# Performance work log

Measured on AMD Instinct MI355X. Metric: run time of the kernel, lower is better.

## Reference

```python
import jax, jax.numpy as jnp
from jax import lax
import numpy as np

S, B = 512, 128
D_MODEL = 512
HID = 256
NUM_LAYERS = 2
VOCAB_SRC = 30000
N_TAGS = 32


def setup_inputs() -> dict:
    key = jax.random.key(0)
    ks = jax.random.split(key, 10)
    s = 0.05
    return {
        "source": jax.random.randint(ks[0], (S, B), 0, VOCAB_SRC),
        "target": jax.random.randint(ks[1], (S, B), 0, N_TAGS),
        "emb": jax.random.normal(ks[2], (VOCAB_SRC, D_MODEL), jnp.float32) * s,
        # stacked LSTM weights: [layer, direction, 4H, in] (in == D_MODEL == 2*HID)
        "W_ih": jax.random.normal(ks[3], (NUM_LAYERS, 2, 4 * HID, D_MODEL), jnp.float32) * s,
        "W_hh": jax.random.normal(ks[4], (NUM_LAYERS, 2, 4 * HID, HID), jnp.float32) * s,
        "b_ih": jax.random.normal(ks[5], (NUM_LAYERS, 2, 4 * HID), jnp.float32) * s,
        "b_hh": jax.random.normal(ks[6], (NUM_LAYERS, 2, 4 * HID), jnp.float32) * s,
        "W_lin": jax.random.normal(ks[7], (N_TAGS, 2 * HID), jnp.float32) * s,
        "b_lin": jax.random.normal(ks[8], (N_TAGS,), jnp.float32) * s,
        "transition": jax.random.uniform(ks[9], (N_TAGS, N_TAGS), jnp.float32),
    }


def _lstm_dir(x, Wih, Whh, bias, reverse):
    # x: [S,B,I]; pre-compute input contribution once
    Bsz = x.shape[1]
    H = Whh.shape[1]
    pre = jnp.einsum('sbi,gi->sbg', x, Wih) + bias  # [S,B,4H]

    def cell(carry, p):
        h, c = carry
        gates = p + h @ Whh.T
        i, f, g, o = jnp.split(gates, 4, axis=-1)  # PyTorch gate order i,f,g,o
        c = jax.nn.sigmoid(f) * c + jax.nn.sigmoid(i) * jnp.tanh(g)
        h = jax.nn.sigmoid(o) * jnp.tanh(c)
        return (h, c), h

    init = (jnp.zeros((Bsz, H), x.dtype), jnp.zeros((Bsz, H), x.dtype))
    _, hs = lax.scan(cell, init, pre, reverse=reverse)
    return hs  # [S,B,H] in original time order


def _forward(source, target, emb, W_ih, W_hh, b_ih, b_hh, W_lin, b_lin, transition):
    d = emb.shape[1]
    x = emb[source] * jnp.sqrt(jnp.asarray(d, jnp.float32))  # [S,B,D]
    for l in range(NUM_LAYERS):
        fwd = _lstm_dir(x, W_ih[l, 0], W_hh[l, 0], b_ih[l, 0] + b_hh[l, 0], reverse=False)
        bwd = _lstm_dir(x, W_ih[l, 1], W_hh[l, 1], b_ih[l, 1] + b_hh[l, 1], reverse=True)
        x = jnp.concatenate([fwd, bwd], axis=-1)  # [S,B,2H]
    logits = jnp.einsum('sbh,th->sbt', x, W_lin) + b_lin  # [S,B,T]

    # CRF partition function: alpha recurrence with fused logsumexp
    def step(alpha, e):
        # alpha: [B,T]; transition[j,k] from j->k; e: emissions at step i [B,T]
        alpha = jax.nn.logsumexp(alpha[:, :, None] + transition[None, :, :], axis=1) + e
        return alpha, None

    alpha, _ = lax.scan(step, logits[0], logits[1:])
    log_z = jax.nn.logsumexp(alpha, axis=1)  # [B]

    # gold path score
    em = jnp.take_along_axis(logits, target[:, :, None], axis=2)[..., 0].sum(axis=0)  # [B]
    tr = transition[target[:-1], target[1:]].sum(axis=0)  # [B]
    return jnp.mean(log_z - em - tr)


def reference(source, target, emb, W_ih, W_hh, b_ih, b_hh, W_lin, b_lin, transition):
    return _forward(source, target, emb, W_ih, W_hh, b_ih, b_hh, W_lin, b_lin, transition)
```

## Files before the change

### kernel.cpp

```cpp
#include <hip/hip_runtime.h>
#include <math.h>

typedef __attribute__((ext_vector_type(8))) short short8;
typedef __attribute__((ext_vector_type(4))) float float4v;
typedef __attribute__((ext_vector_type(8))) int int8v;
typedef unsigned short ushort_t;
typedef unsigned char uchar_t;

#define S_LEN 512
#define BATCH 128
#define DMODEL 512
#define HIDDEN 256
#define NTAGS 32
#define MROWS (S_LEN*BATCH)
#define CHUNK 128
#define NCH (S_LEN/CHUNK)
#define EMB_SCALE 22.62741699796952f

__device__ __forceinline__ float bf2f(ushort_t u){
  union { unsigned int i; float f; } v; v.i = ((unsigned int)u)<<16; return v.f;
}
__device__ __forceinline__ ushort_t f2bf(float f){
  union { float f; unsigned int i; } v; v.f = f;
  unsigned int x = v.i;
  x += 0x7fffu + ((x>>16)&1u);
  return (ushort_t)(x>>16);
}
__device__ __forceinline__ uchar_t f2fp8(float f){
  float a = fabsf(f);
  unsigned int s = (__float_as_uint(f) >> 24) & 0x80u;
  if (a >= 448.f) return (uchar_t)(s | 0x7Eu);
  if (a < 0.015625f){
    unsigned int q = (unsigned int)__float2int_rn(a * 512.0f);
    return (uchar_t)(s | q);
  }
  unsigned int x = __float_as_uint(a);
  x += 0x7FFFFu + ((x >> 20) & 1u);
  int e = (int)((x >> 23) & 0xFFu) - 127;
  unsigned int m = (x >> 20) & 7u;
  if (e > 8) return (uchar_t)(s | 0x7Eu);
  return (uchar_t)(s | ((unsigned)(e + 7) << 3) | m);
}
__device__ __forceinline__ float sigm(float x){ return 1.0f/(1.0f+__expf(-x)); }
__device__ __forceinline__ float tanh_f(float x){ return 2.0f/(1.0f+__expf(-2.0f*x)) - 1.0f; }

#define MFMA(a,b,c) __builtin_amdgcn_mfma_f32_16x16x32_bf16(a,b,c,0,0,0)
#define MFMAMX(a,b,c) __builtin_amdgcn_mfma_scale_f32_16x16x128_f8f6f4( \
    a, b, c, 0, 0, 0, 0x7F7F7F7F, 0, 0x7F7F7F7F)

typedef const __attribute__((address_space(1))) void gas_void;
typedef __attribute__((address_space(3))) void las_void;
__device__ __forceinline__ void gload16(const void* g, void* l){
  __builtin_amdgcn_global_load_lds((gas_void*)g, (las_void*)l, 16, 0, 0);
}

__global__ void k_cvt_bf16(const float* __restrict__ s, ushort_t* __restrict__ d, int n){
  int i = blockIdx.x*blockDim.x + threadIdx.x;
  if(i<n) d[i] = f2bf(s[i]);
}
__global__ void k_cvt_fp8p(const float* __restrict__ s, uchar_t* __restrict__ d, int n){
  int i = blockIdx.x*blockDim.x + threadIdx.x;
  if(i<n){
    int row = i >> 8, q = i & 255;
    int u = ((q >> 5) << 5) + ((q & 1) << 4) + ((q >> 1) & 15);
    d[i] = f2fp8(s[row*256 + u]);
  }
}
__global__ void k_biassum(const float* __restrict__ a, const float* __restrict__ b,
                          float* __restrict__ o, int n){
  int i = blockIdx.x*blockDim.x + threadIdx.x;
  if(i<n) o[i] = a[i]+b[i];
}

__global__ __launch_bounds__(64) void k_embed(const int* __restrict__ src,
                                              const float* __restrict__ emb,
                                              ushort_t* __restrict__ x){
  int row = blockIdx.x;
  int t = threadIdx.x;
  int tok = src[row];
  const float4v* e = (const float4v*)(emb + (size_t)tok*DMODEL + t*8);
  float4v a = e[0], b = e[1];
  short8 o;
  o[0]=(short)f2bf(a[0]*EMB_SCALE); o[1]=(short)f2bf(a[1]*EMB_SCALE);
  o[2]=(short)f2bf(a[2]*EMB_SCALE); o[3]=(short)f2bf(a[3]*EMB_SCALE);
  o[4]=(short)f2bf(b[0]*EMB_SCALE); o[5]=(short)f2bf(b[1]*EMB_SCALE);
  o[6]=(short)f2bf(b[2]*EMB_SCALE); o[7]=(short)f2bf(b[3]*EMB_SCALE);
  *(short8*)(x + (size_t)row*DMODEL + t*8) = o;
}

__global__ __launch_bounds__(256) void k_gemm_band(
    const ushort_t* __restrict__ xin, int t0,
    const ushort_t* __restrict__ WihL,
    const float* __restrict__ bsumL,
    ushort_t* __restrict__ outF,
    ushort_t* __restrict__ outB){
  __shared__ __align__(16) uchar_t smem[32768];
  uchar_t* As = smem;
  uchar_t* Bs = smem + 16384;
  int tid = threadIdx.x;
  int tu = blockIdx.x;
  int by = blockIdx.y;
  int dir = by >> 7, bm = by & 127;
  const uchar_t* Ab = (const uchar_t*)(xin +
      (size_t)(dir ? (S_LEN - t0 - CHUNK) : t0)*BATCH*DMODEL +
      (size_t)bm*128*DMODEL);
  const uchar_t* Wb = (const uchar_t*)(WihL + (size_t)dir*1024*DMODEL);
  ushort_t* Cb = dir ? outB : outF;
  const float* bb = bsumL + dir*1024;

  int lane = tid & 63, w = tid >> 6;
  int wm = w >> 1, wn = w & 1;
  int r = lane & 15, hi = lane >> 4;
  int srow = tid >> 3;
  int sslot = (tid & 7) * 16;
  float4v acc[4][4] = {};

  for(int kt=0; kt<8; ++kt){
    #pragma unroll
    for(int i=0;i<4;++i){
      int row = i*32 + srow;
      int src = sslot ^ ((row & 7) << 4);
      gload16(Ab + (size_t)row*1024 + (size_t)kt*128 + src,
              As + i*4096 + w*1024);
      gload16(Wb + (size_t)(i*256 + tu*32 + srow)*1024 + (size_t)kt*128 + src,
              Bs + i*4096 + w*1024);
    }
    __syncthreads();
    #pragma unroll
    for(int ks=0; ks<2; ++ks){
      int kb = ks*64 + hi*16;
      short8 af[4], bf[4];
      #pragma unroll
      for(int m=0;m<4;++m){
        int row = wm*64 + m*16 + r;
        af[m] = *(const short8*)(As + row*128 + (kb ^ ((row&7)<<4)));
      }
      #pragma unroll
      for(int n=0;n<4;++n){
        int row = wn*64 + n*16 + r;
        bf[n] = *(const short8*)(Bs + row*128 + (kb ^ ((row&7)<<4)));
      }
      #pragma unroll
      for(int m=0;m<4;++m)
        #pragma unroll
        for(int n=0;n<4;++n)
          acc[m][n] = MFMA(af[m], bf[n], acc[m][n]);
    }
    __syncthreads();
  }
  uchar_t* Cs = smem;
  int cc = lane & 15;
  #pragma unroll
  for(int n=0;n<4;++n){
    int rb = wn*64 + n*16 + cc;
    int g = rb >> 5, ul = rb & 31;
    int cl = (ul << 2) | g;
    float bv = bb[g*256 + tu*32 + ul];
    #pragma unroll
    for(int m=0;m<4;++m){
      #pragma unroll
      for(int j=0;j<4;++j){
        int row = wm*64 + m*16 + hi*4 + j;
        *(ushort_t*)&Cs[row*256 + ((cl*2) ^ ((row&7)<<4))] =
            f2bf(acc[m][n][j] + bv);
      }
    }
  }
  __syncthreads();
  #pragma unroll
  for(int p=0;p<8;++p){
    int idx = p*4096 + tid*16;
    int row = idx >> 8, cb = idx & 255;
    short8 v = *(const short8*)&Cs[row*256 + (cb ^ ((row&7)<<4))];
    *(short8*)&Cb[(size_t)(bm*128 + row)*1024 + tu*128 + (cb>>1)] = v;
  }
}

__global__ __launch_bounds__(512,1) void k_scan3(
    const ushort_t* __restrict__ preF,
    const ushort_t* __restrict__ preB,
    const uchar_t* __restrict__ Wq,
    uchar_t* __restrict__ hstate,
    float* __restrict__ cstate,
    ushort_t* __restrict__ xout,
    int t0){
  __shared__ __align__(16) uchar_t hbuf[2][288];
  int bid = blockIdx.x;
  int d = bid >> 7, b = bid & 127;
  int tid = threadIdx.x;
  int w = tid >> 6, lane = tid & 63;
  int lo = lane & 15, hi = lane >> 4;
  int u0 = w*32;

  if(tid < 64)
    *(unsigned int*)&hbuf[0][tid*4] =
      *(const unsigned int*)(hstate + ((size_t)d*BATCH + b)*HIDDEN + tid*4);

  int8v wq[4][2][2];
  const uchar_t* Wd = Wq + (size_t)d*1024*HIDDEN;
  #pragma unroll
  for(int g=0; g<4; ++g)
    #pragma unroll
    for(int uh=0; uh<2; ++uh)
      #pragma unroll
      for(int kt=0; kt<2; ++kt)
        wq[g][uh][kt] = *(const int8v*)
          (Wd + (size_t)(g*256 + u0 + uh*16 + lo)*HIDDEN + kt*128 + hi*32);

  float c[2];
  #pragma unroll
  for(int uh=0; uh<2; ++uh)
    c[uh] = cstate[((size_t)d*BATCH + b)*HIDDEN + u0 + uh*16 + lo];

  const ushort_t* pp = (d ? preB : preF) + (size_t)b*1024;
  ushort4 pc[2], pn[2];
  {
    int br = d ? (CHUNK-1) : 0;
    if(hi==0){
      #pragma unroll
      for(int uh=0; uh<2; ++uh)
        pc[uh] = *(const ushort4*)(pp + (size_t)br*BATCH*1024 + (u0+uh*16+lo)*4);
    }
  }
  __syncthreads();

  for(int sb=0; sb<CHUNK; ++sb){
    int p = sb & 1;
    int sb2 = (sb+1 < CHUNK) ? sb+1 : sb;
    int br2 = d ? (CHUNK-1-sb2) : sb2;
    if(hi==0){
      #pragma unroll
      for(int uh=0; uh<2; ++uh)
        pn[uh] = *(const ushort4*)(pp + (size_t)br2*BATCH*1024 + (u0+uh*16+lo)*4);
    }

    int8v ha0 = {0,0,0,0,0,0,0,0};
    int8v ha1 = {0,0,0,0,0,0,0,0};
    if(lo==0){
      ha0 = *(const int8v*)&hbuf[p][hi*32];
      ha1 = *(const int8v*)&hbuf[p][128 + hi*32];
    }
    float4v acc[4][2] = {};
    #pragma unroll
    for(int g=0; g<4; ++g){
      acc[g][0] = MFMAMX(ha0, wq[g][0][0], acc[g][0]);
      acc[g][1] = MFMAMX(ha0, wq[g][1][0], acc[g][1]);
      acc[g][0] = MFMAMX(ha1, wq[g][0][1], acc[g][0]);
      acc[g][1] = MFMAMX(ha1, wq[g][1][1], acc[g][1]);
    }

    int s = t0 + sb;
    int s_eff = d ? (S_LEN-1-s) : s;
    if(hi==0){
      float hnv[2];
      #pragma unroll
      for(int uh=0; uh<2; ++uh){
        float gi = acc[0][uh][0] + bf2f(pc[uh].x);
        float gf = acc[1][uh][0] + bf2f(pc[uh].y);
        float gg = acc[2][uh][0] + bf2f(pc[uh].z);
        float go = acc[3][uh][0] + bf2f(pc[uh].w);
        float cn = sigm(gf)*c[uh] + sigm(gi)*tanh_f(gg);
        float hn = sigm(go)*tanh_f(cn);
        c[uh] = cn;
        hnv[uh] = hn;
        int u = u0 + uh*16 + lo;
        xout[((size_t)s_eff*BATCH + b)*DMODEL + d*HIDDEN + u] = f2bf(hn);
      }
#if __has_builtin(__builtin_amdgcn_cvt_pk_fp8_f32)
      int pk = __builtin_amdgcn_cvt_pk_fp8_f32(hnv[0], hnv[1], 0, false);
      *(ushort_t*)&hbuf[p^1][u0 + 2*lo] = (ushort_t)pk;
#else
      hbuf[p^1][u0 + 2*lo]     = f2fp8(hnv[0]);
      hbuf[p^1][u0 + 2*lo + 1] = f2fp8(hnv[1]);
#endif
    }
    asm volatile("s_waitcnt lgkmcnt(0)\n\ts_barrier" ::: "memory");
    #pragma unroll
    for(int uh=0; uh<2; ++uh) pc[uh] = pn[uh];
  }

  if(tid < 64)
    *(unsigned int*)(hstate + ((size_t)d*BATCH + b)*HIDDEN + tid*4) =
      *(const unsigned int*)&hbuf[0][tid*4];
  if(hi==0){
    #pragma unroll
    for(int uh=0; uh<2; ++uh)
      cstate[((size_t)d*BATCH + b)*HIDDEN + u0 + uh*16 + lo] = c[uh];
  }
}

__global__ __launch_bounds__(256) void k_logits(const ushort_t* __restrict__ x,
                                                const ushort_t* __restrict__ Wl,
                                                const float* __restrict__ bl,
                                                float* __restrict__ logits){
  int tid = threadIdx.x;
  int lane = tid & 63, w = tid >> 6;
  int rowb = blockIdx.x*64 + w*16;
  int r = lane & 15, hi = lane >> 4;
  float4v acc[2] = {};
  #pragma unroll
  for(int kt=0; kt<16; ++kt){
    short8 a  = *(const short8*)&x [(size_t)(rowb + r)*DMODEL + kt*32 + hi*8];
    short8 b0 = *(const short8*)&Wl[(size_t)(r     )*DMODEL + kt*32 + hi*8];
    short8 b1 = *(const short8*)&Wl[(size_t)(16 + r)*DMODEL + kt*32 + hi*8];
    acc[0] = MFMA(a, b0, acc[0]);
    acc[1] = MFMA(a, b1, acc[1]);
  }
  #pragma unroll
  for(int nt=0; nt<2; ++nt){
    float bv = bl[nt*16 + r];
    #pragma unroll
    for(int j=0; j<4; ++j)
      logits[(size_t)(rowb + hi*4 + j)*NTAGS + nt*16 + r] = acc[nt][j] + bv;
  }
}

__global__ __launch_bounds__(64) void k_crf(const float* __restrict__ logits,
                                            const float* __restrict__ trans,
                                            float* __restrict__ logz){
  __shared__ __align__(16) float sh[32];
  int b = blockIdx.x, tid = threadIdx.x;
  int t = tid & 31;

  float eT[32];
  #pragma unroll
  for(int j=0;j<32;++j) eT[j] = __expf(trans[j*NTAGS + t]);

  float al0 = logits[(size_t)b*NTAGS + t];
  float m0 = al0;
  #pragma unroll
  for(int o=1;o<32;o<<=1) m0 = fmaxf(m0, __shfl_xor(m0, o));
  float Mf = m0;
  float a = __expf(al0 - m0);

  const size_t stp = (size_t)BATCH*NTAGS;
  const float* ebase = logits + (size_t)b*NTAGS + t;
  float eCur = ebase[stp*1];
  float eNxt = ebase[stp*2];
  const float* eptr = ebase + stp*3;

  for(int i=1;i<S_LEN;++i){
    float expE = __expf(eCur);
    if(tid < 32) sh[t] = a;
    __syncthreads();
    float eP = 0.f;
    if(i+2 < S_LEN) eP = *eptr;
    eptr += stp;
    float s0=0.f, s1=0.f, s2=0.f, s3=0.f;
    const float4v* s4 = (const float4v*)sh;
    #pragma unroll
    for(int q=0;q<8;++q){
      float4v v = s4[q];
      s0 = __fmaf_rn(v[0], eT[q*4+0], s0);
      s1 = __fmaf_rn(v[1], eT[q*4+1], s1);
      s2 = __fmaf_rn(v[2], eT[q*4+2], s2);
      s3 = __fmaf_rn(v[3], eT[q*4+3], s3);
    }
    a = ((s0+s1)+(s2+s3)) * expE;
    eCur = eNxt; eNxt = eP;
    if(__any(a > 1.1529215e18f) || __all(a < 9.0949470e-13f)){
      float m = a;
      #pragma unroll
      for(int o=1;o<32;o<<=1) m = fmaxf(m, __shfl_xor(m, o));
      int e2 = (int)((__float_as_uint(m)>>23)&255u) - 127;
      float scl = __uint_as_float((unsigned)(127 - e2) << 23);
      a *= scl;
      Mf += (float)e2 * 0.69314718055994531f;
    }
    __syncthreads();
  }
  float sum = a;
  #pragma unroll
  for(int o=1;o<32;o<<=1) sum += __shfl_xor(sum, o);
  if(tid==0) logz[b] = Mf + __logf(sum);
}

__global__ __launch_bounds__(256) void k_gold(const float* __restrict__ logits,
                                              const int* __restrict__ tgt,
                                              const float* __restrict__ trans,
                                              const float* __restrict__ logz,
                                              float* __restrict__ partial){
  int b = blockIdx.x, tid = threadIdx.x;
  float local = 0.f;
  for(int s=tid; s<S_LEN; s+=256){
    int ts = tgt[s*BATCH + b];
    local += logits[((size_t)s*BATCH + b)*NTAGS + ts];
    if(s > 0){
      int tp = tgt[(s-1)*BATCH + b];
      local += trans[tp*NTAGS + ts];
    }
  }
  __shared__ float red[4];
  for(int o=32;o>0;o>>=1) local += __shfl_down(local, o, 64);
  if((tid&63)==0) red[tid>>6] = local;
  __syncthreads();
  if(tid==0) partial[b] = logz[b] - (red[0]+red[1]+red[2]+red[3]);
}
__global__ __launch_bounds__(128) void k_final(const float* __restrict__ partial,
                                               float* __restrict__ out){
  int t = threadIdx.x;
  float v = partial[t];
  for(int o=32;o>0;o>>=1) v += __shfl_down(v, o, 64);
  __shared__ float r2[2];
  if((t&63)==0) r2[t>>6] = v;
  __syncthreads();
  if(t==0) out[0] = (r2[0]+r2[1]) * (1.0f/BATCH);
}

extern "C" void kernel_launch(void* const* d_in, const int* in_sizes, int n_in,
                              void* d_out, int out_size, void* d_ws, size_t ws_size,
                              hipStream_t stream){
  const int*   src   = (const int*)d_in[0];
  const int*   tgt   = (const int*)d_in[1];
  const float* emb   = (const float*)d_in[2];
  const float* Wih   = (const float*)d_in[3];
  const float* Whh   = (const float*)d_in[4];
  const float* bih   = (const float*)d_in[5];
  const float* bhh   = (const float*)d_in[6];
  const float* Wlin  = (const float*)d_in[7];
  const float* blin  = (const float*)d_in[8];
  const float* trans = (const float*)d_in[9];
  float* out = (float*)d_out;
  char* ws = (char*)d_ws;

  ushort_t* xA     = (ushort_t*)(ws + 0);
  ushort_t* xB     = (ushort_t*)(ws + 67108864);
  ushort_t* preF   = (ushort_t*)(ws + 134217728);
  ushort_t* preB   = (ushort_t*)(ws + 167772160);
  ushort_t* WihB   = (ushort_t*)(ws + 201326592);
  uchar_t*  Wq8    = (uchar_t*) (ws + 205520896);
  ushort_t* WlinB  = (ushort_t*)(ws + 206569472);
  float*    bsum   = (float*)   (ws + 206602240);
  uchar_t*  hstate = (uchar_t*) (ws + 206618624);
  float*    cstate = (float*)   (ws + 206684160);
  float*    logz   = (float*)   (ws + 206946304);
  float*    partial= (float*)   (ws + 206946816);
  float*    logits = (float*)   (ws + 134217728);

  k_cvt_bf16<<<dim3(8192),dim3(256),0,stream>>>(Wih,  WihB,  2*2*1024*512);
  k_cvt_fp8p<<<dim3(4096),dim3(256),0,stream>>>(Whh,  Wq8,   2*2*1024*256);
  k_cvt_bf16<<<dim3(64),  dim3(256),0,stream>>>(Wlin, WlinB, 32*512);
  k_biassum <<<dim3(16),  dim3(256),0,stream>>>(bih, bhh, bsum, 2*2*1024);

  k_embed<<<dim3(MROWS),dim3(64),0,stream>>>(src, emb, xA);

  for(int l=0;l<2;++l){
    const ushort_t* xin = l ? xB : xA;
    ushort_t*      xo   = l ? xA : xB;
    hipMemsetAsync(hstate, 0, 65536 + 262144, stream);
    const uchar_t*  WqL   = Wq8  + (size_t)l*2*1024*HIDDEN;
    const ushort_t* WihL  = WihB + (size_t)l*2*1024*DMODEL;
    const float*    bsumL = bsum + l*2*1024;
    for(int c=0;c<NCH;++c){
      int t0 = c*CHUNK;
      k_gemm_band<<<dim3(8, 256),dim3(256),0,stream>>>(
          xin, t0, WihL, bsumL, preF, preB);
      k_scan3<<<dim3(256),dim3(512),0,stream>>>(
          preF, preB, WqL, hstate, cstate, xo, t0);
    }
  }

  k_logits<<<dim3(MROWS/64),dim3(256),0,stream>>>(xA, WlinB, blin, logits);
  k_crf   <<<dim3(BATCH),dim3(64),0,stream>>>(logits, trans, logz);
  k_gold  <<<dim3(BATCH),dim3(256),0,stream>>>(logits, tgt, trans, logz, partial);
  k_final <<<dim3(1),dim3(128),0,stream>>>(partial, out);
}
```

Before: 2.126 ms.

## Overlap next-chunk input GEMM with LSTM scan in one fused launch

Merges the per-chunk input-projection GEMM and the recurrent scan into a single kernel. The first 256 blocks run the sequential LSTM scan on the current chunk while the extra blocks compute the next chunk's pre-activations into a double-buffered band. Only the first band is computed by a standalone GEMM launch. The chunk size is halved to shorten the serial prologue, at the cost of more launches and co-scheduling contention between GEMM and scan blocks.

Measured after the change: 2.296 ms. +8.0%, slower.

```diff
diff --git a/kernel.cpp b/kernel.cpp
--- a/kernel.cpp
+++ b/kernel.cpp
@@ -13,7 +13,7 @@
 #define HIDDEN 256
 #define NTAGS 32
 #define MROWS (S_LEN*BATCH)
-#define CHUNK 128
+#define CHUNK 64
 #define NCH (S_LEN/CHUNK)
 #define EMB_SCALE 22.62741699796952f
 
@@ -99,8 +99,8 @@
   uchar_t* Bs = smem + 16384;
   int tid = threadIdx.x;
   int tu = blockIdx.x;
-  int by = blockIdx.y;
-  int dir = by >> 7, bm = by & 127;
+  int bm = blockIdx.y;
+  int dir = blockIdx.z;
   const uchar_t* Ab = (const uchar_t*)(xin +
       (size_t)(dir ? (S_LEN - t0 - CHUNK) : t0)*BATCH*DMODEL +
       (size_t)bm*128*DMODEL);
@@ -176,116 +176,207 @@
   }
 }
 
-__global__ __launch_bounds__(512,1) void k_scan3(
+__global__ __launch_bounds__(512,1) void k_scan_gemm(
     const ushort_t* __restrict__ preF,
     const ushort_t* __restrict__ preB,
     const uchar_t* __restrict__ Wq,
     uchar_t* __restrict__ hstate,
     float* __restrict__ cstate,
     ushort_t* __restrict__ xout,
-    int t0){
-  __shared__ __align__(16) uchar_t hbuf[2][288];
+    int t0,
+    const ushort_t* __restrict__ xin,
+    const ushort_t* __restrict__ WihL,
+    const float* __restrict__ bsumL,
+    ushort_t* __restrict__ outF,
+    ushort_t* __restrict__ outB,
+    int t0n){
+  __shared__ __align__(16) uchar_t smem[32768];
   int bid = blockIdx.x;
-  int d = bid >> 7, b = bid & 127;
   int tid = threadIdx.x;
-  int w = tid >> 6, lane = tid & 63;
-  int lo = lane & 15, hi = lane >> 4;
-  int u0 = w*32;
-
-  if(tid < 64)
-    *(unsigned int*)&hbuf[0][tid*4] =
-      *(const unsigned int*)(hstate + ((size_t)d*BATCH + b)*HIDDEN + tid*4);
-
-  int8v wq[4][2][2];
-  const uchar_t* Wd = Wq + (size_t)d*1024*HIDDEN;
-  #pragma unroll
-  for(int g=0; g<4; ++g)
+
+  if(bid < 256){
+    uchar_t (*hbuf)[288] = (uchar_t(*)[288])smem;
+    int d = bid >> 7, b = bid & 127;
+    int w = tid >> 6, lane = tid & 63;
+    int lo = lane & 15, hi = lane >> 4;
+    int u0 = w*32;
+
+    if(tid < 64)
+      *(unsigned int*)&hbuf[0][tid*4] =
+        *(const unsigned int*)(hstate + ((size_t)d*BATCH + b)*HIDDEN + tid*4);
+
+    int8v wq[4][2][2];
+    const uchar_t* Wd = Wq + (size_t)d*1024*HIDDEN;
+    #pragma unroll
+    for(int g=0; g<4; ++g)
+      #pragma unroll
+      for(int uh=0; uh<2; ++uh)
+        #pragma unroll
+        for(int kt=0; kt<2; ++kt)
+          wq[g][uh][kt] = *(const int8v*)
+            (Wd + (size_t)(g*256 + u0 + uh*16 + lo)*HIDDEN + kt*128 + hi*32);
+
+    float c[2];
     #pragma unroll
     for(int uh=0; uh<2; ++uh)
-      #pragma unroll
-      for(int kt=0; kt<2; ++kt)
-        wq[g][uh][kt] = *(const int8v*)
-          (Wd + (size_t)(g*256 + u0 + uh*16 + lo)*HIDDEN + kt*128 + hi*32);
-
-  float c[2];
-  #pragma unroll
-  for(int uh=0; uh<2; ++uh)
-    c[uh] = cstate[((size_t)d*BATCH + b)*HIDDEN + u0 + uh*16 + lo];
-
-  const ushort_t* pp = (d ? preB : preF) + (size_t)b*1024;
-  ushort4 pc[2], pn[2];
-  {
-    int br = d ? (CHUNK-1) : 0;
+      c[uh] = cstate[((size_t)d*BATCH + b)*HIDDEN + u0 + uh*16 + lo];
+
+    const ushort_t* pp = (d ? preB : preF) + (size_t)b*1024;
+    ushort4 pc[2], pn[2];
+    {
+      int br = d ? (CHUNK-1) : 0;
+      if(hi==0){
+        #pragma unroll
+        for(int uh=0; uh<2; ++uh)
+          pc[uh] = *(const ushort4*)(pp + (size_t)br*BATCH*1024 + (u0+uh*16+lo)*4);
+      }
+    }
+    __syncthreads();
+
+    for(int sb=0; sb<CHUNK; ++sb){
+      int p = sb & 1;
+      int sb2 = (sb+1 < CHUNK) ? sb+1 : sb;
+      int br2 = d ? (CHUNK-1-sb2) : sb2;
+      if(hi==0){
+        #pragma unroll
+        for(int uh=0; uh<2; ++uh)
+          pn[uh] = *(const ushort4*)(pp + (size_t)br2*BATCH*1024 + (u0+uh*16+lo)*4);
+      }
+
+      int8v ha0 = {0,0,0,0,0,0,0,0};
+      int8v ha1 = {0,0,0,0,0,0,0,0};
+      if(lo==0){
+        ha0 = *(const int8v*)&hbuf[p][hi*32];
+        ha1 = *(const int8v*)&hbuf[p][128 + hi*32];
+      }
+      float4v acc[4][2] = {};
+      #pragma unroll
+      for(int g=0; g<4; ++g){
+        acc[g][0] = MFMAMX(ha0, wq[g][0][0], acc[g][0]);
+        acc[g][1] = MFMAMX(ha0, wq[g][1][0], acc[g][1]);
+        acc[g][0] = MFMAMX(ha1, wq[g][0][1], acc[g][0]);
+        acc[g][1] = MFMAMX(ha1, wq[g][1][1], acc[g][1]);
+      }
+
+      int s = t0 + sb;
+      int s_eff = d ? (S_LEN-1-s) : s;
+      if(hi==0){
+        float hnv[2];
+        #pragma unroll
+        for(int uh=0; uh<2; ++uh){
+          float gi = acc[0][uh][0] + bf2f(pc[uh].x);
+          float gf = acc[1][uh][0] + bf2f(pc[uh].y);
+          float gg = acc[2][uh][0] + bf2f(pc[uh].z);
+          float go = acc[3][uh][0] + bf2f(pc[uh].w);
+          float cn = sigm(gf)*c[uh] + sigm(gi)*tanh_f(gg);
+          float hn = sigm(go)*tanh_f(cn);
+          c[uh] = cn;
+          hnv[uh] = hn;
+          int u = u0 + uh*16 + lo;
+          xout[((size_t)s_eff*BATCH + b)*DMODEL + d*HIDDEN + u] = f2bf(hn);
+        }
+#if __has_builtin(__builtin_amdgcn_cvt_pk_fp8_f32)
+        int pk = __builtin_amdgcn_cvt_pk_fp8_f32(hnv[0], hnv[1], 0, false);
+        *(ushort_t*)&hbuf[p^1][u0 + 2*lo] = (ushort_t)pk;
+#else
+        hbuf[p^1][u0 + 2*lo]     = f2fp8(hnv[0]);
+        hbuf[p^1][u0 + 2*lo + 1] = f2fp8(hnv[1]);
+#endif
+      }
+      asm volatile("s_waitcnt lgkmcnt(0)\n\ts_barrier" ::: "memory");
+      #pragma unroll
+      for(int uh=0; uh<2; ++uh) pc[uh] = pn[uh];
+    }
+
+    if(tid < 64)
+      *(unsigned int*)(hstate + ((size_t)d*BATCH + b)*HIDDEN + tid*4) =
+        *(const unsigned int*)&hbuf[0][tid*4];
     if(hi==0){
       #pragma unroll
       for(int uh=0; uh<2; ++uh)
-        pc[uh] = *(const ushort4*)(pp + (size_t)br*BATCH*1024 + (u0+uh*16+lo)*4);
-    }
-  }
-  __syncthreads();
-
-  for(int sb=0; sb<CHUNK; ++sb){
-    int p = sb & 1;
-    int sb2 = (sb+1 < CHUNK) ? sb+1 : sb;
-    int br2 = d ? (CHUNK-1-sb2) : sb2;
-    if(hi==0){
-      #pragma unroll
-      for(int uh=0; uh<2; ++uh)
-        pn[uh] = *(const ushort4*)(pp + (size_t)br2*BATCH*1024 + (u0+uh*16+lo)*4);
-    }
-
-    int8v ha0 = {0,0,0,0,0,0,0,0};
-    int8v ha1 = {0,0,0,0,0,0,0,0};
-    if(lo==0){
-      ha0 = *(const int8v*)&hbuf[p][hi*32];
-      ha1 = *(const int8v*)&hbuf[p][128 + hi*32];
-    }
+        cstate[((size_t)d*BATCH + b)*HIDDEN + u0 + uh*16 + lo] = c[uh];
+    }
+  } else {
+    int gid = bid - 256;
+    int tu  = gid & 7;
+    int rest = gid >> 3;
+    int dir = rest >> 6, bm = rest & 63;
+    uchar_t* As = smem;
+    uchar_t* Bs = smem + 16384;
+    const uchar_t* Ab = (const uchar_t*)(xin +
+        (size_t)(dir ? (S_LEN - t0n - CHUNK) : t0n)*BATCH*DMODEL +
+        (size_t)bm*128*DMODEL);
+    const uchar_t* Wb = (const uchar_t*)(WihL + (size_t)dir*1024*DMODEL);
+    ushort_t* Cb = dir ? outB : outF;
+    const float* bb = bsumL + dir*1024;
+
+    int lane = tid & 63, w = tid >> 6;
+    int wm = w >> 2, wn = w & 3;
+    int r = lane & 15, hi = lane >> 4;
+    int srow = tid >> 3;
+    int sslot = (tid & 7) * 16;
     float4v acc[4][2] = {};
-    #pragma unroll
-    for(int g=0; g<4; ++g){
-      acc[g][0] = MFMAMX(ha0, wq[g][0][0], acc[g][0]);
-      acc[g][1] = MFMAMX(ha0, wq[g][1][0], acc[g][1]);
-      acc[g][0] = MFMAMX(ha1, wq[g][0][1], acc[g][0]);
-      acc[g][1] = MFMAMX(ha1, wq[g][1][1], acc[g][1]);
-    }
-
-    int s = t0 + sb;
-    int s_eff = d ? (S_LEN-1-s) : s;
-    if(hi==0){
-      float hnv[2];
-      #pragma unroll
-      for(int uh=0; uh<2; ++uh){
-        float gi = acc[0][uh][0] + bf2f(pc[uh].x);
-        float gf = acc[1][uh][0] + bf2f(pc[uh].y);
-        float gg = acc[2][uh][0] + bf2f(pc[uh].z);
-        float go = acc[3][uh][0] + bf2f(pc[uh].w);
-        float cn = sigm(gf)*c[uh] + sigm(gi)*tanh_f(gg);
-        float hn = sigm(go)*tanh_f(cn);
-        c[uh] = cn;
-        hnv[uh] = hn;
-        int u = u0 + uh*16 + lo;
-        xout[((size_t)s_eff*BATCH + b)*DMODEL + d*HIDDEN + u] = f2bf(hn);
-      }
-#if __has_builtin(__builtin_amdgcn_cvt_pk_fp8_f32)
-      int pk = __builtin_amdgcn_cvt_pk_fp8_f32(hnv[0], hnv[1], 0, false);
-      *(ushort_t*)&hbuf[p^1][u0 + 2*lo] = (ushort_t)pk;
-#else
-      hbuf[p^1][u0 + 2*lo]     = f2fp8(hnv[0]);
-      hbuf[p^1][u0 + 2*lo + 1] = f2fp8(hnv[1]);
-#endif
-    }
-    asm volatile("s_waitcnt lgkmcnt(0)\n\ts_barrier" ::: "memory");
-    #pragma unroll
-    for(int uh=0; uh<2; ++uh) pc[uh] = pn[uh];
-  }
-
-  if(tid < 64)
-    *(unsigned int*)(hstate + ((size_t)d*BATCH + b)*HIDDEN + tid*4) =
-      *(const unsigned int*)&hbuf[0][tid*4];
-  if(hi==0){
-    #pragma unroll
-    for(int uh=0; uh<2; ++uh)
-      cstate[((size_t)d*BATCH + b)*HIDDEN + u0 + uh*16 + lo] = c[uh];
+
+    for(int kt=0; kt<8; ++kt){
+      #pragma unroll
+      for(int i=0;i<2;++i){
+        int row = i*64 + srow;
+        int src = sslot ^ ((row & 7) << 4);
+        gload16(Ab + (size_t)row*1024 + (size_t)kt*128 + src,
+                As + i*8192 + w*1024);
+        gload16(Wb + (size_t)((row>>5)*256 + tu*32 + (row&31))*1024
+                   + (size_t)kt*128 + src,
+                Bs + i*8192 + w*1024);
+      }
+      __syncthreads();
+      #pragma unroll
+      for(int ks=0; ks<2; ++ks){
+        int kb = ks*64 + hi*16;
+        short8 af[4], bf[2];
+        #pragma unroll
+        for(int m=0;m<4;++m){
+          int row = wm*64 + m*16 + r;
+          af[m] = *(const short8*)(As + row*128 + (kb ^ ((row&7)<<4)));
+        }
+        #pragma unroll
+        for(int n=0;n<2;++n){
+          int row = wn*32 + n*16 + r;
+          bf[n] = *(const short8*)(Bs + row*128 + (kb ^ ((row&7)<<4)));
+        }
+        #pragma unroll
+        for(int m=0;m<4;++m)
+          #pragma unroll
+          for(int n=0;n<2;++n)
+            acc[m][n] = MFMA(af[m], bf[n], acc[m][n]);
+      }
+      __syncthreads();
+    }
+    uchar_t* Cs = smem;
+    int cc = lane & 15;
+    #pragma unroll
+    for(int n=0;n<2;++n){
+      int rb = wn*32 + n*16 + cc;
+      int g = rb >> 5, ul = rb & 31;
+      int cl = (ul << 2) | g;
+      float bv = bb[g*256 + tu*32 + ul];
+      #pragma unroll
+      for(int m=0;m<4;++m){
+        #pragma unroll
+        for(int j=0;j<4;++j){
+          int row = wm*64 + m*16 + hi*4 + j;
+          *(ushort_t*)&Cs[row*256 + ((cl*2) ^ ((row&7)<<4))] =
+              f2bf(acc[m][n][j] + bv);
+        }
+      }
+    }
+    __syncthreads();
+    #pragma unroll
+    for(int p=0;p<4;++p){
+      int idx = p*8192 + tid*16;
+      int row = idx >> 8, cb = idx & 255;
+      short8 v = *(const short8*)&Cs[row*256 + (cb ^ ((row&7)<<4))];
+      *(short8*)&Cb[(size_t)(bm*128 + row)*1024 + tu*128 + (cb>>1)] = v;
+    }
   }
 }
 
@@ -423,10 +514,12 @@
   float* out = (float*)d_out;
   char* ws = (char*)d_ws;
 
+  const size_t BSZ = (size_t)CHUNK*BATCH*1024*sizeof(ushort_t);
   ushort_t* xA     = (ushort_t*)(ws + 0);
   ushort_t* xB     = (ushort_t*)(ws + 67108864);
-  ushort_t* preF   = (ushort_t*)(ws + 134217728);
-  ushort_t* preB   = (ushort_t*)(ws + 167772160);
+  char*     bands  =             ws + 134217728;
+  ushort_t* bF[2]  = { (ushort_t*)(bands),           (ushort_t*)(bands + 2*BSZ) };
+  ushort_t* bB[2]  = { (ushort_t*)(bands + BSZ),     (ushort_t*)(bands + 3*BSZ) };
   ushort_t* WihB   = (ushort_t*)(ws + 201326592);
   uchar_t*  Wq8    = (uchar_t*) (ws + 205520896);
   ushort_t* WlinB  = (ushort_t*)(ws + 206569472);
@@ -451,12 +544,15 @@
     const uchar_t*  WqL   = Wq8  + (size_t)l*2*1024*HIDDEN;
     const ushort_t* WihL  = WihB + (size_t)l*2*1024*DMODEL;
     const float*    bsumL = bsum + l*2*1024;
+    k_gemm_band<<<dim3(8, CHUNK*BATCH/128, 2),dim3(256),0,stream>>>(
+        xin, 0, WihL, bsumL, bF[0], bB[0]);
     for(int c=0;c<NCH;++c){
+      int par = c & 1;
       int t0 = c*CHUNK;
-      k_gemm_band<<<dim3(8, 256),dim3(256),0,stream>>>(
-          xin, t0, WihL, bsumL, preF, preB);
-      k_scan3<<<dim3(256),dim3(512),0,stream>>>(
-          preF, preB, WqL, hstate, cstate, xo, t0);
+      int ngem = (c+1 < NCH) ? 1 : 0;
+      k_scan_gemm<<<dim3(ngem ? 1280 : 256),dim3(512),0,stream>>>(
+          bF[par], bB[par], WqL, hstate, cstate, xo, t0,
+          xin, WihL, bsumL, bF[par^1], bB[par^1], t0 + CHUNK);
     }
   }
 
```
